# Optimization experiments

Hardware: AMD Instinct MI355X
Metric: run time of the kernel (lower is better)

Reference implementation:

```python
import jax, jax.numpy as jnp
import numpy as np

# Network geometry: 8 layers x 524288 buckets, 8 spigots per bucket (uniform).
L_LAYERS = 8
B_PER_LAYER = 524288
NB = L_LAYERS * B_PER_LAYER      # total buckets = 4_194_304
NS = 8                           # spigots per bucket
G = 9.8                          # gravity constant from module


def setup_inputs() -> dict:
    key = jax.random.key(0)
    k1, k2, k3, k4 = jax.random.split(key, 4)
    # Head starts above all spigot heights (initial_head_in_buckets ~ 2) so h > 0.
    H = 2.0 + jax.random.uniform(k1, (NB,), dtype=jnp.float32)
    # S[..., 0] = spigot height in (0,1); S[..., 1] = spigot area in (0,1).
    S = jax.random.uniform(k2, (NB, NS, 2), dtype=jnp.float32)
    # theta flattened in (layer, bucket, spigot) order -> plain reshape to [NB, NS].
    theta = jax.random.uniform(k3, (NB * NS,), dtype=jnp.float32)
    # precip_into_network_at_update (scalar), unit_precip = 6.0 scale.
    precip = jax.random.uniform(k4, (), dtype=jnp.float32) * 6.0
    return {"H": H, "S": S, "theta": theta, "precip": precip}


def reference(H, S, theta, precip):
    # --- update_spigot_outflow (vectorized over layers/buckets/spigots) ---
    th = theta.reshape(NB, NS)                      # triple loop == reshape
    h = jnp.maximum(0.0, H[:, None] - S[:, :, 0])   # head above spigot
    flow_rate_modifier = 0.5 * (jnp.tanh(h) + 1.0)
    v = th * jnp.sqrt(2.0 * G * h) * flow_rate_modifier
    s_q = v * S[:, :, 1]                            # [NB, NS] spigot outflows

    # --- update_network_fluxes (upstream precip distribution) ---
    outflows = jnp.sum(s_q, axis=1)                 # [NB]
    # inflows[1:] = outflows[:-1]; inflows[0] = precip (upstream)
    inflows = jnp.concatenate([precip[None].astype(H.dtype), outflows[:-1]])

    # --- update_head_in_buckets ---
    H_new = H + inflows - outflows

    # --- set_network_outflow: total outflow of last layer's buckets ---
    network_outflow = jnp.sum(s_q[NB - B_PER_LAYER:])

    return H_new, s_q, network_outflow
```

## Files before the change

### kernel.cpp

```cpp
#include <hip/hip_runtime.h>

#define NL 8
#define BPL 524288
#define NB (NL * BPL)
#define NS 8
#define GRAV 9.8f

__global__ __launch_bounds__(256) void spigot_kernel(
    const float* __restrict__ H,
    const float* __restrict__ S,
    const float* __restrict__ theta,
    float* __restrict__ s_q,
    float* __restrict__ outflows)
{
    const int tid    = blockIdx.x * 256 + threadIdx.x;
    const int bucket = tid >> 3;

    const float  th = theta[tid];
    const float2 sv = reinterpret_cast<const float2*>(S)[tid];
    const float  Hb = H[bucket];

    const float h   = fmaxf(0.0f, Hb - sv.x);
    const float e   = __expf(-2.0f * h);
    const float mod = __builtin_amdgcn_rcpf(1.0f + e);
    const float v   = th * __builtin_amdgcn_sqrtf(2.0f * GRAV * h) * mod;
    const float q   = v * sv.y;

    s_q[tid] = q;

    if (outflows != nullptr) {
        float sum = q;
        sum += __shfl_xor(sum, 1);
        sum += __shfl_xor(sum, 2);
        sum += __shfl_xor(sum, 4);
        if ((threadIdx.x & 7) == 0) outflows[bucket] = sum;
    }
}

__global__ __launch_bounds__(256) void head_kernel(
    const float* __restrict__ H,
    const float* __restrict__ outflows,
    const float* __restrict__ precip,
    float* __restrict__ H_new,
    float* __restrict__ net_out)
{
    const int t = blockIdx.x * 256 + threadIdx.x;
    const int i = t << 2;

    const float4 o  = reinterpret_cast<const float4*>(outflows)[t];
    const float4 Hv = reinterpret_cast<const float4*>(H)[t];
    const float om1 = (i == 0) ? precip[0] : outflows[i - 1];

    float4 hn;
    hn.x = Hv.x + om1 - o.x;
    hn.y = Hv.y + o.x - o.y;
    hn.z = Hv.z + o.y - o.z;
    hn.w = Hv.w + o.z - o.w;
    reinterpret_cast<float4*>(H_new)[t] = hn;

    float part = (o.x + o.y) + (o.z + o.w);
    part += __shfl_xor(part, 1);
    part += __shfl_xor(part, 2);
    part += __shfl_xor(part, 4);
    part += __shfl_xor(part, 8);
    part += __shfl_xor(part, 16);
    part += __shfl_xor(part, 32);

    __shared__ float smem[4];
    const int lane = threadIdx.x & 63;
    const int w    = threadIdx.x >> 6;
    if (lane == 0) smem[w] = part;
    __syncthreads();
    if (threadIdx.x == 0 && blockIdx.x >= ((NB - BPL) >> 10)) {
        atomicAdd(net_out, (smem[0] + smem[1]) + (smem[2] + smem[3]));
    }
}

__global__ __launch_bounds__(256) void head_kernel_nows(
    const float* __restrict__ H,
    const float* __restrict__ s_q,
    const float* __restrict__ precip,
    float* __restrict__ H_new,
    float* __restrict__ net_out)
{
    const int i = blockIdx.x * 256 + threadIdx.x;
    const float4* q4 = reinterpret_cast<const float4*>(s_q);

    const float4 a = q4[i * 2];
    const float4 b = q4[i * 2 + 1];
    const float of = ((a.x + a.y) + (a.z + a.w)) + ((b.x + b.y) + (b.z + b.w));

    float infl;
    if (i == 0) {
        infl = precip[0];
    } else {
        const float4 c = q4[i * 2 - 2];
        const float4 d = q4[i * 2 - 1];
        infl = ((c.x + c.y) + (c.z + c.w)) + ((d.x + d.y) + (d.z + d.w));
    }
    H_new[i] = H[i] + infl - of;

    float part = (i >= NB - BPL) ? of : 0.0f;
    part += __shfl_xor(part, 1);
    part += __shfl_xor(part, 2);
    part += __shfl_xor(part, 4);
    part += __shfl_xor(part, 8);
    part += __shfl_xor(part, 16);
    part += __shfl_xor(part, 32);

    __shared__ float smem[4];
    const int lane = threadIdx.x & 63;
    const int w    = threadIdx.x >> 6;
    if (lane == 0) smem[w] = part;
    __syncthreads();
    if (threadIdx.x == 0 && blockIdx.x >= ((NB - BPL) >> 8)) {
        atomicAdd(net_out, (smem[0] + smem[1]) + (smem[2] + smem[3]));
    }
}

extern "C" void kernel_launch(void* const* d_in, const int* in_sizes, int n_in,
                              void* d_out, int out_size, void* d_ws, size_t ws_size,
                              hipStream_t stream) {
    const float* H      = (const float*)d_in[0];
    const float* S      = (const float*)d_in[1];
    const float* theta  = (const float*)d_in[2];
    const float* precip = (const float*)d_in[3];

    float* out     = (float*)d_out;
    float* H_new   = out;
    float* s_q     = out + NB;
    float* net_out = out + NB + (size_t)NB * NS;

    hipMemsetAsync(net_out, 0, sizeof(float), stream);

    const bool have_ws = (ws_size >= (size_t)NB * sizeof(float));
    float* outflows = have_ws ? (float*)d_ws : nullptr;

    spigot_kernel<<<(NB * NS) / 256, 256, 0, stream>>>(H, S, theta, s_q, outflows);

    if (have_ws) {
        head_kernel<<<NB / 1024, 256, 0, stream>>>(H, outflows, precip, H_new, net_out);
    } else {
        head_kernel_nows<<<NB / 256, 256, 0, stream>>>(H, s_q, precip, H_new, net_out);
    }
}
```

Measured before the change: 489.2 us.

## Fuse spigot and head kernels into one per-bucket kernel with halo recompute

Merges the spigot outflow computation and the head update into a single kernel where each thread handles one bucket's eight spigots with vectorized float4 loads. The upstream inflow crosses wave boundaries via shuffle and shared memory, and each block's first bucket inflow is recomputed from the previous bucket. This removes the outflows workspace round trip and a second launch, at the cost of a strided per-thread access pattern and a small redundant computation per block.

```diff
diff --git a/kernel.cpp b/kernel.cpp
--- a/kernel.cpp
+++ b/kernel.cpp
@@ -5,116 +5,100 @@
 #define NB (NL * BPL)
 #define NS 8
 #define GRAV 9.8f
+#define BUCKETS_PER_BLOCK 256
+#define LAST_BLOCK0 ((NB - BPL) / BUCKETS_PER_BLOCK)
 
-__global__ __launch_bounds__(256) void spigot_kernel(
+__device__ __forceinline__ float spigot_q(float Hb, float sh, float sa, float th) {
+    const float h   = fmaxf(0.0f, Hb - sh);
+    const float e   = __expf(-2.0f * h);
+    const float mod = __builtin_amdgcn_rcpf(1.0f + e);
+    return th * __builtin_amdgcn_sqrtf(2.0f * GRAV * h) * mod * sa;
+}
+
+__global__ __launch_bounds__(256) void fused_kernel(
     const float* __restrict__ H,
     const float* __restrict__ S,
     const float* __restrict__ theta,
-    float* __restrict__ s_q,
-    float* __restrict__ outflows)
-{
-    const int tid    = blockIdx.x * 256 + threadIdx.x;
-    const int bucket = tid >> 3;
-
-    const float  th = theta[tid];
-    const float2 sv = reinterpret_cast<const float2*>(S)[tid];
-    const float  Hb = H[bucket];
-
-    const float h   = fmaxf(0.0f, Hb - sv.x);
-    const float e   = __expf(-2.0f * h);
-    const float mod = __builtin_amdgcn_rcpf(1.0f + e);
-    const float v   = th * __builtin_amdgcn_sqrtf(2.0f * GRAV * h) * mod;
-    const float q   = v * sv.y;
-
-    s_q[tid] = q;
-
-    if (outflows != nullptr) {
-        float sum = q;
-        sum += __shfl_xor(sum, 1);
-        sum += __shfl_xor(sum, 2);
-        sum += __shfl_xor(sum, 4);
-        if ((threadIdx.x & 7) == 0) outflows[bucket] = sum;
-    }
-}
-
-__global__ __launch_bounds__(256) void head_kernel(
-    const float* __restrict__ H,
-    const float* __restrict__ outflows,
     const float* __restrict__ precip,
     float* __restrict__ H_new,
+    float* __restrict__ s_q,
     float* __restrict__ net_out)
 {
-    const int t = blockIdx.x * 256 + threadIdx.x;
-    const int i = t << 2;
+    const int b    = blockIdx.x * BUCKETS_PER_BLOCK + threadIdx.x;
+    const int lane = threadIdx.x & 63;
+    const int wv   = threadIdx.x >> 6;
 
-    const float4 o  = reinterpret_cast<const float4*>(outflows)[t];
-    const float4 Hv = reinterpret_cast<const float4*>(H)[t];
-    const float om1 = (i == 0) ? precip[0] : outflows[i - 1];
+    __shared__ float s_last[4];
+    __shared__ float s_bp;
+    __shared__ float s_part[4];
 
-    float4 hn;
-    hn.x = Hv.x + om1 - o.x;
-    hn.y = Hv.y + o.x - o.y;
-    hn.z = Hv.z + o.y - o.z;
-    hn.w = Hv.w + o.z - o.w;
-    reinterpret_cast<float4*>(H_new)[t] = hn;
+    const float4* th4 = reinterpret_cast<const float4*>(theta);
+    const float4* sv4 = reinterpret_cast<const float4*>(S);
+    const float4 t0 = th4[b * 2 + 0];
+    const float4 t1 = th4[b * 2 + 1];
+    const float4 sA = sv4[b * 4 + 0];
+    const float4 sB = sv4[b * 4 + 1];
+    const float4 sC = sv4[b * 4 + 2];
+    const float4 sD = sv4[b * 4 + 3];
+    const float  Hb = H[b];
 
-    float part = (o.x + o.y) + (o.z + o.w);
-    part += __shfl_xor(part, 1);
-    part += __shfl_xor(part, 2);
-    part += __shfl_xor(part, 4);
-    part += __shfl_xor(part, 8);
-    part += __shfl_xor(part, 16);
-    part += __shfl_xor(part, 32);
+    float4 qA, qB;
+    qA.x = spigot_q(Hb, sA.x, sA.y, t0.x);
+    qA.y = spigot_q(Hb, sA.z, sA.w, t0.y);
+    qA.z = spigot_q(Hb, sB.x, sB.y, t0.z);
+    qA.w = spigot_q(Hb, sB.z, sB.w, t0.w);
+    qB.x = spigot_q(Hb, sC.x, sC.y, t1.x);
+    qB.y = spigot_q(Hb, sC.z, sC.w, t1.y);
+    qB.z = spigot_q(Hb, sD.x, sD.y, t1.z);
+    qB.w = spigot_q(Hb, sD.z, sD.w, t1.w);
 
-    __shared__ float smem[4];
-    const int lane = threadIdx.x & 63;
-    const int w    = threadIdx.x >> 6;
-    if (lane == 0) smem[w] = part;
+    reinterpret_cast<float4*>(s_q)[b * 2 + 0] = qA;
+    reinterpret_cast<float4*>(s_q)[b * 2 + 1] = qB;
+
+    const float of = ((qA.x + qA.y) + (qA.z + qA.w)) +
+                     ((qB.x + qB.y) + (qB.z + qB.w));
+
+    if (lane == 63) s_last[wv] = of;
+
+    if (threadIdx.x < 8) {
+        if (blockIdx.x == 0) {
+            if (threadIdx.x == 0) s_bp = precip[0];
+        } else {
+            const int pb = blockIdx.x * BUCKETS_PER_BLOCK - 1;
+            const int sp = pb * NS + threadIdx.x;
+            const float2 sv = reinterpret_cast<const float2*>(S)[sp];
+            float q = spigot_q(H[pb], sv.x, sv.y, theta[sp]);
+            q += __shfl_xor(q, 1);
+            q += __shfl_xor(q, 2);
+            q += __shfl_xor(q, 4);
+            if (threadIdx.x == 0) s_bp = q;
+        }
+    }
     __syncthreads();
-    if (threadIdx.x == 0 && blockIdx.x >= ((NB - BPL) >> 10)) {
-        atomicAdd(net_out, (smem[0] + smem[1]) + (smem[2] + smem[3]));
+
+    const float up = __shfl_up(of, 1);
+    float prev;
+    if (lane == 0) {
+        prev = (wv == 0) ? s_bp : s_last[wv - 1];
+    } else {
+        prev = up;
     }
-}
 
-__global__ __launch_bounds__(256) void head_kernel_nows(
-    const float* __restrict__ H,
-    const float* __restrict__ s_q,
-    const float* __restrict__ precip,
-    float* __restrict__ H_new,
-    float* __restrict__ net_out)
-{
-    const int i = blockIdx.x * 256 + threadIdx.x;
-    const float4* q4 = reinterpret_cast<const float4*>(s_q);
+    H_new[b] = Hb + prev - of;
 
-    const float4 a = q4[i * 2];
-    const float4 b = q4[i * 2 + 1];
-    const float of = ((a.x + a.y) + (a.z + a.w)) + ((b.x + b.y) + (b.z + b.w));
-
-    float infl;
-    if (i == 0) {
-        infl = precip[0];
-    } else {
-        const float4 c = q4[i * 2 - 2];
-        const float4 d = q4[i * 2 - 1];
-        infl = ((c.x + c.y) + (c.z + c.w)) + ((d.x + d.y) + (d.z + d.w));
-    }
-    H_new[i] = H[i] + infl - of;
-
-    float part = (i >= NB - BPL) ? of : 0.0f;
-    part += __shfl_xor(part, 1);
-    part += __shfl_xor(part, 2);
-    part += __shfl_xor(part, 4);
-    part += __shfl_xor(part, 8);
-    part += __shfl_xor(part, 16);
-    part += __shfl_xor(part, 32);
-
-    __shared__ float smem[4];
-    const int lane = threadIdx.x & 63;
-    const int w    = threadIdx.x >> 6;
-    if (lane == 0) smem[w] = part;
-    __syncthreads();
-    if (threadIdx.x == 0 && blockIdx.x >= ((NB - BPL) >> 8)) {
-        atomicAdd(net_out, (smem[0] + smem[1]) + (smem[2] + smem[3]));
+    if (blockIdx.x >= LAST_BLOCK0) {
+        float p = of;
+        p += __shfl_xor(p, 1);
+        p += __shfl_xor(p, 2);
+        p += __shfl_xor(p, 4);
+        p += __shfl_xor(p, 8);
+        p += __shfl_xor(p, 16);
+        p += __shfl_xor(p, 32);
+        if (lane == 0) s_part[wv] = p;
+        __syncthreads();
+        if (threadIdx.x == 0) {
+            atomicAdd(net_out, (s_part[0] + s_part[1]) + (s_part[2] + s_part[3]));
+        }
     }
 }
 
@@ -133,14 +117,6 @@
 
     hipMemsetAsync(net_out, 0, sizeof(float), stream);
 
-    const bool have_ws = (ws_size >= (size_t)NB * sizeof(float));
-    float* outflows = have_ws ? (float*)d_ws : nullptr;
-
-    spigot_kernel<<<(NB * NS) / 256, 256, 0, stream>>>(H, S, theta, s_q, outflows);
-
-    if (have_ws) {
-        head_kernel<<<NB / 1024, 256, 0, stream>>>(H, outflows, precip, H_new, net_out);
-    } else {
-        head_kernel_nows<<<NB / 256, 256, 0, stream>>>(H, s_q, precip, H_new, net_out);
-    }
+    fused_kernel<<<NB / BUCKETS_PER_BLOCK, 256, 0, stream>>>(
+        H, S, theta, precip, H_new, s_q, net_out);
 }
```

Result: no change. 498.5 us (+1.9%).
